# Kernel tuning notes

Hardware: AMD Instinct MI355X
Metric: run time of the kernel (lower is better)

## Reference

```python
import jax, jax.numpy as jnp
import numpy as np

N_NODES = 50000
N_EDGES = 800000
N_GRAPHS = 256
D_IN, D_H1, D_H2, D_OUT = 64, 64, 64, 64


def gcn_conv(x, W, b, src, dst, n_nodes):
    # PyG GCNConv (eval): h = x @ W; add self-loops; deg[i] = in_deg(i) + 1;
    # out[i] = sum_{j->i} h[j] * deg[i]^-1/2 deg[j]^-1/2 + h[i]/deg[i] + b
    h = x @ W  # [N, F]
    ones = jnp.ones((src.shape[0],), dtype=x.dtype)
    deg = jax.ops.segment_sum(ones, dst, num_segments=n_nodes) + 1.0  # self loop
    dinv = jax.lax.rsqrt(deg)
    norm = dinv[src] * dinv[dst]  # [E]
    msg = h[src] * norm[:, None]  # [E, F]  (memory-bound gather)
    agg = jax.ops.segment_sum(msg, dst, num_segments=n_nodes)  # scatter-add
    agg = agg + h * (1.0 / deg)[:, None]  # self-loop contribution
    return agg + b


def setup_inputs() -> dict:
    key = jax.random.key(0)
    ks = jax.random.split(key, 12)
    x = jax.random.normal(ks[0], (N_NODES, D_IN), dtype=jnp.float32)
    src = jax.random.randint(ks[1], (N_EDGES,), 0, N_NODES)
    dst = jax.random.randint(ks[2], (N_EDGES,), 0, N_NODES)
    batch = jnp.sort(jax.random.randint(ks[3], (N_NODES,), 0, N_GRAPHS))
    def glorot(k, fin, fout):
        s = jnp.sqrt(6.0 / (fin + fout))
        return jax.random.uniform(k, (fin, fout), jnp.float32, -s, s)
    return {
        "x": x, "src": src, "dst": dst, "batch": batch,
        "W1": glorot(ks[4], D_IN, D_H1), "b1": jnp.zeros((D_H1,), jnp.float32),
        "W2": glorot(ks[5], D_H1, D_H2), "b2": jnp.zeros((D_H2,), jnp.float32),
        "W3": glorot(ks[6], D_H2, D_OUT), "b3": jnp.zeros((D_OUT,), jnp.float32),
        "Wl": glorot(ks[7], D_OUT, 1), "bl": jnp.zeros((1,), jnp.float32),
    }


def reference(x, src, dst, batch, W1, b1, W2, b2, W3, b3, Wl, bl):
    n = x.shape[0]
    h = jax.nn.relu(gcn_conv(x, W1, b1, src, dst, n))   # dropout inactive (eval)
    h = jax.nn.relu(gcn_conv(h, W2, b2, src, dst, n))
    h = jax.nn.relu(gcn_conv(h, W3, b3, src, dst, n))
    # global_mean_pool over graph ids
    sums = jax.ops.segment_sum(h, batch, num_segments=N_GRAPHS)  # [G, F]
    cnt = jax.ops.segment_sum(jnp.ones((n,), h.dtype), batch, num_segments=N_GRAPHS)
    pooled = sums / jnp.maximum(cnt, 1.0)[:, None]
    return pooled @ Wl + bl  # [G, 1]
```

## Files before the change

### kernel.cpp

```cpp
#include <hip/hip_runtime.h>

#define N_NODES 50000
#define N_EDGES 800000
#define N_GRAPHS 256
#define F 64
#define NBUCK 196
#define CAP 5120
#define P3_TILE 2048
#define P3_GRID ((N_EDGES + P3_TILE - 1) / P3_TILE)
#define BCAP 6144
#define ZOFF (N_NODES * 128)

__device__ __forceinline__ unsigned short f2bf(float f) {
    union { float f; unsigned u; } c; c.f = f;
    unsigned u = c.u + 0x7FFFu + ((c.u >> 16) & 1u);
    return (unsigned short)(u >> 16);
}
__device__ __forceinline__ unsigned pack2bf(float lo, float hi) {
    return (unsigned)f2bf(lo) | ((unsigned)f2bf(hi) << 16);
}
__device__ __forceinline__ float bfl(unsigned u) {
    union { unsigned u; float f; } c; c.u = u << 16; return c.f;
}
__device__ __forceinline__ float bfh(unsigned u) {
    union { unsigned u; float f; } c; c.u = u & 0xFFFF0000u; return c.f;
}

__device__ __forceinline__ void gather_run(const int* __restrict__ eidx,
                                           const char* __restrict__ Hb,
                                           int beg, int end, int fo, float* a) {
#pragma unroll
    for (int i = 0; i < 8; ++i) a[i] = 0.f;
    int kb = (beg < end) ? beg : 0;
    int4 oc = *(const int4*)(eidx + kb);
    int k1 = beg + 4;
    int k1c = (k1 < end) ? k1 : kb;
    int4 on = *(const int4*)(eidx + k1c);
    uint4 pc = *(const uint4*)(Hb + oc.x + fo);
    uint4 qc = *(const uint4*)(Hb + oc.y + fo);
    uint4 rc = *(const uint4*)(Hb + oc.z + fo);
    uint4 wc = *(const uint4*)(Hb + oc.w + fo);
    for (int k = beg; k < end; k += 4) {
        int k2 = k + 8;
        int k2c = (k2 < end) ? k2 : kb;
        int4 of = *(const int4*)(eidx + k2c);
        uint4 pn = *(const uint4*)(Hb + on.x + fo);
        uint4 qn = *(const uint4*)(Hb + on.y + fo);
        uint4 rn = *(const uint4*)(Hb + on.z + fo);
        uint4 wn = *(const uint4*)(Hb + on.w + fo);
        a[0] += (bfl(pc.x) + bfl(qc.x)) + (bfl(rc.x) + bfl(wc.x));
        a[1] += (bfh(pc.x) + bfh(qc.x)) + (bfh(rc.x) + bfh(wc.x));
        a[2] += (bfl(pc.y) + bfl(qc.y)) + (bfl(rc.y) + bfl(wc.y));
        a[3] += (bfh(pc.y) + bfh(qc.y)) + (bfh(rc.y) + bfh(wc.y));
        a[4] += (bfl(pc.z) + bfl(qc.z)) + (bfl(rc.z) + bfl(wc.z));
        a[5] += (bfh(pc.z) + bfh(qc.z)) + (bfh(rc.z) + bfh(wc.z));
        a[6] += (bfl(pc.w) + bfl(qc.w)) + (bfl(rc.w) + bfl(wc.w));
        a[7] += (bfh(pc.w) + bfh(qc.w)) + (bfh(rc.w) + bfh(wc.w));
        oc = on; on = of;
        pc = pn; qc = qn; rc = rn; wc = wn;
    }
}

__global__ __launch_bounds__(256) void partition_edges(const int* __restrict__ src,
                                                       const int* __restrict__ dst,
                                                       int* __restrict__ bcur,
                                                       unsigned int* __restrict__ bpair) {
    __shared__ int bh[NBUCK], bloc[NBUCK], bpos[NBUCK];
    int t = threadIdx.x;
    int lo = blockIdx.x * P3_TILE;
    int hi = min(lo + P3_TILE, N_EDGES);
    for (int i = t; i < NBUCK; i += 256) { bh[i] = 0; bpos[i] = 0; }
    __syncthreads();
    for (int e = lo + t; e < hi; e += 256) atomicAdd(&bh[dst[e] >> 8], 1);
    __syncthreads();
    for (int i = t; i < NBUCK; i += 256)
        bloc[i] = bh[i] ? atomicAdd(&bcur[i], bh[i]) : 0;
    __syncthreads();
    for (int e = lo + t; e < hi; e += 256) {
        int d = dst[e];
        int b = d >> 8;
        int r = atomicAdd(&bpos[b], 1);
        bpair[(size_t)b * CAP + bloc[b] + r] = ((unsigned)src[e] << 8) | (unsigned)(d & 255);
    }
}

__global__ __launch_bounds__(256) void bucket_sort(const unsigned int* __restrict__ bpair,
                                                   const int* __restrict__ bcur,
                                                   int* __restrict__ eidx,
                                                   int* __restrict__ rbeg,
                                                   int* __restrict__ rend,
                                                   float* __restrict__ dinv,
                                                   unsigned short* __restrict__ Abf,
                                                   unsigned short* __restrict__ Bbf) {
    __shared__ int cnt[256], s[256], pos[256];
    __shared__ int lout[BCAP];
    int b = blockIdx.x, t = threadIdx.x;
    int base = b * CAP;
    int sz = bcur[b];

    if (b == 0 && t < 8) {
        ((uint4*)Abf)[(size_t)N_NODES * 8 + t] = make_uint4(0u, 0u, 0u, 0u);
        ((uint4*)Bbf)[(size_t)N_NODES * 8 + t] = make_uint4(0u, 0u, 0u, 0u);
    }

    cnt[t] = 0;
    __syncthreads();
    for (int i = t; i < sz; i += 256) atomicAdd(&cnt[bpair[base + i] & 255], 1);
    __syncthreads();
    int v = cnt[t];
    int pv = (v + 3) & ~3;
    s[t] = pv;
    __syncthreads();
    for (int off = 1; off < 256; off <<= 1) {
        int u = (t >= off) ? s[t - off] : 0;
        __syncthreads();
        s[t] += u;
        __syncthreads();
    }
    int excl = s[t] - pv;
    pos[t] = excl;
    int node = b * 256 + t;
    if (node < N_NODES) {
        rbeg[node] = base + excl;
        rend[node] = base + excl + pv;
        dinv[node] = 1.0f / sqrtf((float)v + 1.0f);
    }
    int padtot = s[255];
    __syncthreads();

    for (int i = t; i < sz; i += 256) {
        unsigned p = bpair[base + i];
        int r = atomicAdd(&pos[p & 255], 1);
        lout[r] = (int)((p >> 8) << 7);
    }
    __syncthreads();
    for (int j = v; j < pv; j++) lout[excl + j] = ZOFF;
    __syncthreads();
    for (int i = t; i < padtot; i += 256) eidx[base + i] = lout[i];
}

#define XSTRIDE 17
__global__ __launch_bounds__(256) void gemm64_f32(const float* __restrict__ X,
                                                  const float* __restrict__ W,
                                                  const float* __restrict__ dinv,
                                                  unsigned short* __restrict__ Hn, int n) {
    __shared__ float4 sW[64 * 16];
    __shared__ float4 sX[128 * XSTRIDE];
    int tid = threadIdx.x;
    int base = blockIdx.x * 128;

    const float4* W4 = (const float4*)W;
    for (int i = tid; i < 64 * 16; i += 256) sW[i] = W4[i];
    {
        const float4* X4 = (const float4*)X;
        for (int i = tid; i < 128 * 16; i += 256) {
            int r = i >> 4, kg = i & 15;
            int node = base + r;
            sX[r * XSTRIDE + kg] = (node < n) ? X4[(size_t)node * 16 + kg]
                                              : make_float4(0.f, 0.f, 0.f, 0.f);
        }
    }
    __syncthreads();

    int fg = tid & 15;
    int ng = tid >> 4;
    float4 acc[8];
#pragma unroll
    for (int ii = 0; ii < 8; ii++) acc[ii] = make_float4(0.f, 0.f, 0.f, 0.f);

    for (int kg = 0; kg < 16; kg++) {
        float4 xv[8];
#pragma unroll
        for (int ii = 0; ii < 8; ii++) xv[ii] = sX[(ng + 16 * ii) * XSTRIDE + kg];
#pragma unroll
        for (int kk = 0; kk < 4; kk++) {
            float4 wv = sW[(4 * kg + kk) * 16 + fg];
#pragma unroll
            for (int ii = 0; ii < 8; ii++) {
                float xs = (kk == 0) ? xv[ii].x : (kk == 1) ? xv[ii].y
                         : (kk == 2) ? xv[ii].z : xv[ii].w;
                acc[ii].x += wv.x * xs;
                acc[ii].y += wv.y * xs;
                acc[ii].z += wv.z * xs;
                acc[ii].w += wv.w * xs;
            }
        }
    }

    ushort4* H4 = (ushort4*)Hn;
#pragma unroll
    for (int ii = 0; ii < 8; ii++) {
        int node = base + ng + 16 * ii;
        if (node < n) {
            float d = dinv[node];
            float4 o = acc[ii];
            ushort4 u;
            u.x = f2bf(o.x * d); u.y = f2bf(o.y * d);
            u.z = f2bf(o.z * d); u.w = f2bf(o.w * d);
            H4[(size_t)node * 16 + fg] = u;
        }
    }
}

__global__ __launch_bounds__(256) void gather_gemm(const int* __restrict__ rbeg,
                                                   const int* __restrict__ rend,
                                                   const int* __restrict__ eidx,
                                                   const float* __restrict__ dinv,
                                                   const unsigned short* __restrict__ Hin,
                                                   const float* __restrict__ bias,
                                                   const float* __restrict__ W,
                                                   unsigned short* __restrict__ Hout, int n) {
    __shared__ float4 sW[64 * 16];
    const float4* W4 = (const float4*)W;
    for (int i = threadIdx.x; i < 64 * 16; i += 256) sW[i] = W4[i];
    __syncthreads();

    int wv = (blockIdx.x * blockDim.x + threadIdx.x) >> 6;
    if (wv * 8 >= n) return;
    int lane = threadIdx.x & 63;
    int ns = lane >> 3, f = lane & 7;
    int node = wv * 8 + ns;
    int beg = rbeg[node];
    int end = rend[node];
    const char* Hb = (const char*)Hin;

    float di = dinv[node];
    uint4 hs = *(const uint4*)(Hb + (size_t)node * 128 + f * 16);
    float4 bb0 = ((const float4*)bias)[2 * f];
    float4 bb1 = ((const float4*)bias)[2 * f + 1];

    float a[8];
    gather_run(eidx, Hb, beg, end, f * 16, a);

    float v[8];
    v[0] = fmaxf(di * (a[0] + bfl(hs.x)) + bb0.x, 0.f);
    v[1] = fmaxf(di * (a[1] + bfh(hs.x)) + bb0.y, 0.f);
    v[2] = fmaxf(di * (a[2] + bfl(hs.y)) + bb0.z, 0.f);
    v[3] = fmaxf(di * (a[3] + bfh(hs.y)) + bb0.w, 0.f);
    v[4] = fmaxf(di * (a[4] + bfl(hs.z)) + bb1.x, 0.f);
    v[5] = fmaxf(di * (a[5] + bfh(hs.z)) + bb1.y, 0.f);
    v[6] = fmaxf(di * (a[6] + bfl(hs.w)) + bb1.z, 0.f);
    v[7] = fmaxf(di * (a[7] + bfh(hs.w)) + bb1.w, 0.f);

    float y0 = 0.f, y1 = 0.f, y2 = 0.f, y3 = 0.f;
    float y4 = 0.f, y5 = 0.f, y6 = 0.f, y7 = 0.f;
    int pb = (lane & 56) << 2;
#pragma unroll
    for (int c = 0; c < 8; ++c) {
        int ad = pb + 4 * c;
#pragma unroll
        for (int j = 0; j < 8; ++j) {
            float hk = __int_as_float(
                __builtin_amdgcn_ds_bpermute(ad, __float_as_int(v[j])));
            float4 w0 = sW[(8 * c + j) * 16 + 2 * f];
            float4 w1 = sW[(8 * c + j) * 16 + 2 * f + 1];
            y0 += hk * w0.x; y1 += hk * w0.y; y2 += hk * w0.z; y3 += hk * w0.w;
            y4 += hk * w1.x; y5 += hk * w1.y; y6 += hk * w1.z; y7 += hk * w1.w;
        }
    }

    uint4 u;
    u.x = pack2bf(y0 * di, y1 * di);
    u.y = pack2bf(y2 * di, y3 * di);
    u.z = pack2bf(y4 * di, y5 * di);
    u.w = pack2bf(y6 * di, y7 * di);
    ((uint4*)Hout)[(size_t)node * 8 + f] = u;
}

__global__ __launch_bounds__(256) void gather_pool(const int* __restrict__ rbeg,
                                                   const int* __restrict__ rend,
                                                   const int* __restrict__ eidx,
                                                   const float* __restrict__ dinv,
                                                   const unsigned short* __restrict__ Hn,
                                                   const float* __restrict__ b,
                                                   const float* __restrict__ Wl,
                                                   float* __restrict__ pdot, int n) {
    int wv = (blockIdx.x * blockDim.x + threadIdx.x) >> 6;
    int lane = threadIdx.x & 63;
    int ns = lane >> 3, f = lane & 7;
    int node = wv * 8 + ns;
    bool valid = node < n;
    int nodec = valid ? node : 0;
    int beg = valid ? rbeg[node] : 0;
    int end = valid ? rend[node] : 0;
    const char* Hb = (const char*)Hn;

    float di = dinv[nodec];
    uint4 hs = *(const uint4*)(Hb + (size_t)nodec * 128 + f * 16);
    float4 b0 = ((const float4*)b)[2 * f];
    float4 b1 = ((const float4*)b)[2 * f + 1];
    float4 w0 = ((const float4*)Wl)[2 * f];
    float4 w1 = ((const float4*)Wl)[2 * f + 1];

    float a[8];
    gather_run(eidx, Hb, beg, end, f * 16, a);

    float d = 0.f;
    d += fmaxf(di * (a[0] + bfl(hs.x)) + b0.x, 0.f) * w0.x;
    d += fmaxf(di * (a[1] + bfh(hs.x)) + b0.y, 0.f) * w0.y;
    d += fmaxf(di * (a[2] + bfl(hs.y)) + b0.z, 0.f) * w0.z;
    d += fmaxf(di * (a[3] + bfh(hs.y)) + b0.w, 0.f) * w0.w;
    d += fmaxf(di * (a[4] + bfl(hs.z)) + b1.x, 0.f) * w1.x;
    d += fmaxf(di * (a[5] + bfh(hs.z)) + b1.y, 0.f) * w1.y;
    d += fmaxf(di * (a[6] + bfl(hs.w)) + b1.z, 0.f) * w1.z;
    d += fmaxf(di * (a[7] + bfh(hs.w)) + b1.w, 0.f) * w1.w;
#pragma unroll
    for (int m = 1; m <= 4; m <<= 1) d += __shfl_xor(d, m);
    if (valid && f == 0) pdot[node] = d;
}

__global__ __launch_bounds__(64) void final_out(const float* __restrict__ pdot,
                                                const int* __restrict__ batch,
                                                const float* __restrict__ bl,
                                                float* __restrict__ out) {
    int g = blockIdx.x;
    __shared__ int slo, shi;
    int lane = threadIdx.x;
    if (lane == 0) {
        int a = 0, b = N_NODES;
        while (a < b) { int m = (a + b) >> 1; if (batch[m] < g) a = m + 1; else b = m; }
        slo = a;
        b = N_NODES;
        while (a < b) { int m = (a + b) >> 1; if (batch[m] < g + 1) a = m + 1; else b = m; }
        shi = a;
    }
    __syncthreads();
    int lo = slo, hi = shi;
    float acc = 0.f;
    for (int i = lo + lane; i < hi; i += 64) acc += pdot[i];
#pragma unroll
    for (int off = 32; off > 0; off >>= 1) acc += __shfl_down(acc, off);
    if (lane == 0) {
        float cnt = (float)(hi - lo);
        out[g] = acc / fmaxf(cnt, 1.0f) + bl[0];
    }
}

extern "C" void kernel_launch(void* const* d_in, const int* in_sizes, int n_in,
                              void* d_out, int out_size, void* d_ws, size_t ws_size,
                              hipStream_t stream) {
    const float* x     = (const float*)d_in[0];
    const int*   src   = (const int*)d_in[1];
    const int*   dst   = (const int*)d_in[2];
    const int*   batch = (const int*)d_in[3];
    const float* W1 = (const float*)d_in[4];  const float* b1 = (const float*)d_in[5];
    const float* W2 = (const float*)d_in[6];  const float* b2 = (const float*)d_in[7];
    const float* W3 = (const float*)d_in[8];  const float* b3 = (const float*)d_in[9];
    const float* Wl = (const float*)d_in[10]; const float* bl = (const float*)d_in[11];
    float* out = (float*)d_out;

    char* ws = (char*)d_ws;
    unsigned short* Abf = (unsigned short*)ws;
    unsigned short* Bbf = Abf + (size_t)(N_NODES + 1) * F;
    float* dinv    = (float*)(Bbf + (size_t)(N_NODES + 1) * F);
    float* pdot    = dinv + N_NODES;
    int*   rbeg    = (int*)(pdot + N_NODES);
    int*   rend    = rbeg + N_NODES;
    int*   bcur    = rend + N_NODES;
    unsigned int* bpair = (unsigned int*)(bcur + NBUCK);
    int*   eidx    = (int*)(bpair + (size_t)NBUCK * CAP);

    const int GEMM_GRID   = (N_NODES + 127) / 128;
    const int GATHER_GRID = (N_NODES + 31) / 32;

    hipMemsetAsync(bcur, 0, NBUCK * sizeof(int), stream);
    partition_edges<<<P3_GRID, 256, 0, stream>>>(src, dst, bcur, bpair);
    bucket_sort<<<NBUCK, 256, 0, stream>>>(bpair, bcur, eidx, rbeg, rend, dinv, Abf, Bbf);

    gemm64_f32<<<GEMM_GRID, 256, 0, stream>>>(x, W1, dinv, Abf, N_NODES);

    gather_gemm<<<GATHER_GRID, 256, 0, stream>>>(rbeg, rend, eidx, dinv, Abf, b1, W2, Bbf, N_NODES);

    gather_gemm<<<GATHER_GRID, 256, 0, stream>>>(rbeg, rend, eidx, dinv, Bbf, b2, W3, Abf, N_NODES);

    gather_pool<<<GATHER_GRID, 256, 0, stream>>>(rbeg, rend, eidx, dinv, Abf, b3, Wl, pdot, N_NODES);

    final_out<<<N_GRAPHS, 64, 0, stream>>>(pdot, batch, bl, out);
}
```

Before: 194.7 us.

## Reorder nodes by degree within buckets to balance gather wavefront work

The bucket sort now also counting-sorts the 256 nodes in each bucket by padded in-degree and writes an order array. The gather kernels process nodes in that order, so the 8 nodes sharing a wavefront have similar edge counts and less lane divergence and idle time. Padding slots beyond N_NODES are handled with valid guards, which adds some wasted wavefronts in the last bucket. The change also adds an extra indirection load and scattered output writes.

```diff
diff --git a/kernel.cpp b/kernel.cpp
--- a/kernel.cpp
+++ b/kernel.cpp
@@ -10,6 +10,7 @@
 #define P3_GRID ((N_EDGES + P3_TILE - 1) / P3_TILE)
 #define BCAP 6144
 #define ZOFF (N_NODES * 128)
+#define NSLOT (NBUCK * 256)
 
 __device__ __forceinline__ unsigned short f2bf(float f) {
     union { float f; unsigned u; } c; c.f = f;
@@ -90,9 +91,11 @@
                                                    int* __restrict__ rbeg,
                                                    int* __restrict__ rend,
                                                    float* __restrict__ dinv,
+                                                   int* __restrict__ ord,
                                                    unsigned short* __restrict__ Abf,
                                                    unsigned short* __restrict__ Bbf) {
     __shared__ int cnt[256], s[256], pos[256];
+    __shared__ int dhist[64], dscan[64];
     __shared__ int lout[BCAP];
     int b = blockIdx.x, t = threadIdx.x;
     int base = b * CAP;
@@ -104,12 +107,15 @@
     }
 
     cnt[t] = 0;
+    if (t < 64) dhist[t] = 0;
     __syncthreads();
     for (int i = t; i < sz; i += 256) atomicAdd(&cnt[bpair[base + i] & 255], 1);
     __syncthreads();
     int v = cnt[t];
     int pv = (v + 3) & ~3;
     s[t] = pv;
+    int ic = min(pv >> 2, 63);
+    int myoff = atomicAdd(&dhist[ic], 1);
     __syncthreads();
     for (int off = 1; off < 256; off <<= 1) {
         int u = (t >= off) ? s[t - off] : 0;
@@ -126,7 +132,17 @@
         dinv[node] = 1.0f / sqrtf((float)v + 1.0f);
     }
     int padtot = s[255];
-    __syncthreads();
+
+    if (t < 64) dscan[t] = dhist[t];
+    __syncthreads();
+    for (int off = 1; off < 64; off <<= 1) {
+        int u = (t >= off && t < 64) ? dscan[t - off] : 0;
+        __syncthreads();
+        if (t < 64) dscan[t] += u;
+        __syncthreads();
+    }
+    int rank = dscan[ic] - dhist[ic] + myoff;
+    ord[b * 256 + rank] = node;
 
     for (int i = t; i < sz; i += 256) {
         unsigned p = bpair[base + i];
@@ -202,30 +218,32 @@
     }
 }
 
-__global__ __launch_bounds__(256) void gather_gemm(const int* __restrict__ rbeg,
+__global__ __launch_bounds__(256) void gather_gemm(const int* __restrict__ ord,
+                                                   const int* __restrict__ rbeg,
                                                    const int* __restrict__ rend,
                                                    const int* __restrict__ eidx,
                                                    const float* __restrict__ dinv,
                                                    const unsigned short* __restrict__ Hin,
                                                    const float* __restrict__ bias,
                                                    const float* __restrict__ W,
-                                                   unsigned short* __restrict__ Hout, int n) {
+                                                   unsigned short* __restrict__ Hout) {
     __shared__ float4 sW[64 * 16];
     const float4* W4 = (const float4*)W;
     for (int i = threadIdx.x; i < 64 * 16; i += 256) sW[i] = W4[i];
     __syncthreads();
 
     int wv = (blockIdx.x * blockDim.x + threadIdx.x) >> 6;
-    if (wv * 8 >= n) return;
     int lane = threadIdx.x & 63;
     int ns = lane >> 3, f = lane & 7;
-    int node = wv * 8 + ns;
-    int beg = rbeg[node];
-    int end = rend[node];
+    int node = ord[wv * 8 + ns];
+    bool valid = node < N_NODES;
+    int nodec = valid ? node : 0;
+    int beg = valid ? rbeg[nodec] : 0;
+    int end = valid ? rend[nodec] : 0;
     const char* Hb = (const char*)Hin;
 
-    float di = dinv[node];
-    uint4 hs = *(const uint4*)(Hb + (size_t)node * 128 + f * 16);
+    float di = dinv[nodec];
+    uint4 hs = *(const uint4*)(Hb + (size_t)nodec * 128 + f * 16);
     float4 bb0 = ((const float4*)bias)[2 * f];
     float4 bb1 = ((const float4*)bias)[2 * f + 1];
 
@@ -259,33 +277,36 @@
         }
     }
 
-    uint4 u;
-    u.x = pack2bf(y0 * di, y1 * di);
-    u.y = pack2bf(y2 * di, y3 * di);
-    u.z = pack2bf(y4 * di, y5 * di);
-    u.w = pack2bf(y6 * di, y7 * di);
-    ((uint4*)Hout)[(size_t)node * 8 + f] = u;
-}
-
-__global__ __launch_bounds__(256) void gather_pool(const int* __restrict__ rbeg,
+    if (valid) {
+        uint4 u;
+        u.x = pack2bf(y0 * di, y1 * di);
+        u.y = pack2bf(y2 * di, y3 * di);
+        u.z = pack2bf(y4 * di, y5 * di);
+        u.w = pack2bf(y6 * di, y7 * di);
+        ((uint4*)Hout)[(size_t)node * 8 + f] = u;
+    }
+}
+
+__global__ __launch_bounds__(256) void gather_pool(const int* __restrict__ ord,
+                                                   const int* __restrict__ rbeg,
                                                    const int* __restrict__ rend,
                                                    const int* __restrict__ eidx,
                                                    const float* __restrict__ dinv,
                                                    const unsigned short* __restrict__ Hn,
                                                    const float* __restrict__ b,
                                                    const float* __restrict__ Wl,
-                                                   float* __restrict__ pdot, int n) {
+                                                   float* __restrict__ pdot) {
     int wv = (blockIdx.x * blockDim.x + threadIdx.x) >> 6;
     int lane = threadIdx.x & 63;
     int ns = lane >> 3, f = lane & 7;
-    int node = wv * 8 + ns;
-    bool valid = node < n;
+    int node = ord[wv * 8 + ns];
+    bool valid = node < N_NODES;
     int nodec = valid ? node : 0;
-    int beg = valid ? rbeg[node] : 0;
-    int end = valid ? rend[node] : 0;
+    int beg = valid ? rbeg[nodec] : 0;
+    int end = valid ? rend[nodec] : 0;
     const char* Hb = (const char*)Hn;
 
-    float di = dinv[nodec];
+    float di = valid ? dinv[nodec] : 0.f;
     uint4 hs = *(const uint4*)(Hb + (size_t)nodec * 128 + f * 16);
     float4 b0 = ((const float4*)b)[2 * f];
     float4 b1 = ((const float4*)b)[2 * f + 1];
@@ -356,24 +377,25 @@
     float* pdot    = dinv + N_NODES;
     int*   rbeg    = (int*)(pdot + N_NODES);
     int*   rend    = rbeg + N_NODES;
-    int*   bcur    = rend + N_NODES;
+    int*   ord     = rend + N_NODES;
+    int*   bcur    = ord + NSLOT;
     unsigned int* bpair = (unsigned int*)(bcur + NBUCK);
     int*   eidx    = (int*)(bpair + (size_t)NBUCK * CAP);
 
     const int GEMM_GRID   = (N_NODES + 127) / 128;
-    const int GATHER_GRID = (N_NODES + 31) / 32;
+    const int GATHER_GRID = NSLOT / 32;
 
     hipMemsetAsync(bcur, 0, NBUCK * sizeof(int), stream);
     partition_edges<<<P3_GRID, 256, 0, stream>>>(src, dst, bcur, bpair);
-    bucket_sort<<<NBUCK, 256, 0, stream>>>(bpair, bcur, eidx, rbeg, rend, dinv, Abf, Bbf);
+    bucket_sort<<<NBUCK, 256, 0, stream>>>(bpair, bcur, eidx, rbeg, rend, dinv, ord, Abf, Bbf);
 
     gemm64_f32<<<GEMM_GRID, 256, 0, stream>>>(x, W1, dinv, Abf, N_NODES);
 
-    gather_gemm<<<GATHER_GRID, 256, 0, stream>>>(rbeg, rend, eidx, dinv, Abf, b1, W2, Bbf, N_NODES);
-
-    gather_gemm<<<GATHER_GRID, 256, 0, stream>>>(rbeg, rend, eidx, dinv, Bbf, b2, W3, Abf, N_NODES);
-
-    gather_pool<<<GATHER_GRID, 256, 0, stream>>>(rbeg, rend, eidx, dinv, Abf, b3, Wl, pdot, N_NODES);
+    gather_gemm<<<GATHER_GRID, 256, 0, stream>>>(ord, rbeg, rend, eidx, dinv, Abf, b1, W2, Bbf);
+
+    gather_gemm<<<GATHER_GRID, 256, 0, stream>>>(ord, rbeg, rend, eidx, dinv, Bbf, b2, W3, Abf);
+
+    gather_pool<<<GATHER_GRID, 256, 0, stream>>>(ord, rbeg, rend, eidx, dinv, Abf, b3, Wl, pdot);
 
     final_out<<<N_GRAPHS, 64, 0, stream>>>(pdot, batch, bl, out);
 }
```

After: 249.7 us. +28.2%, slower.

## Split each node's edge gather across four lane groups with shuffle reduction

Applied to the files above, without the earlier changes.

The gather kernels now map two nodes per wavefront instead of eight. Four 8-lane groups stride through each node's edge list and their partial sums are combined with cross-lane shuffles, which raises memory-level parallelism per node and cuts the serial per-node loop length. The fused 64x64 GEMM is restructured around a transposed, padded shared weight copy and bf16-packed bpermutes, with each half of the lanes computing half the K range and then reducing. The grid grows fourfold, the bounds check is removed (this relies on N_NODES being divisible by 8), and edge prefetching drops from the 4-wide double-buffered scheme to a single-index lookahead.

```diff
diff --git a/kernel.cpp b/kernel.cpp
--- a/kernel.cpp
+++ b/kernel.cpp
@@ -26,38 +26,24 @@
     union { unsigned u; float f; } c; c.u = u & 0xFFFF0000u; return c.f;
 }
 
-__device__ __forceinline__ void gather_run(const int* __restrict__ eidx,
-                                           const char* __restrict__ Hb,
-                                           int beg, int end, int fo, float* a) {
+__device__ __forceinline__ void gather_run4(const int* __restrict__ eidx,
+                                            const char* __restrict__ Hb,
+                                            int k0, int end, int fo, float* a) {
 #pragma unroll
     for (int i = 0; i < 8; ++i) a[i] = 0.f;
-    int kb = (beg < end) ? beg : 0;
-    int4 oc = *(const int4*)(eidx + kb);
-    int k1 = beg + 4;
-    int k1c = (k1 < end) ? k1 : kb;
-    int4 on = *(const int4*)(eidx + k1c);
-    uint4 pc = *(const uint4*)(Hb + oc.x + fo);
-    uint4 qc = *(const uint4*)(Hb + oc.y + fo);
-    uint4 rc = *(const uint4*)(Hb + oc.z + fo);
-    uint4 wc = *(const uint4*)(Hb + oc.w + fo);
-    for (int k = beg; k < end; k += 4) {
-        int k2 = k + 8;
-        int k2c = (k2 < end) ? k2 : kb;
-        int4 of = *(const int4*)(eidx + k2c);
-        uint4 pn = *(const uint4*)(Hb + on.x + fo);
-        uint4 qn = *(const uint4*)(Hb + on.y + fo);
-        uint4 rn = *(const uint4*)(Hb + on.z + fo);
-        uint4 wn = *(const uint4*)(Hb + on.w + fo);
-        a[0] += (bfl(pc.x) + bfl(qc.x)) + (bfl(rc.x) + bfl(wc.x));
-        a[1] += (bfh(pc.x) + bfh(qc.x)) + (bfh(rc.x) + bfh(wc.x));
-        a[2] += (bfl(pc.y) + bfl(qc.y)) + (bfl(rc.y) + bfl(wc.y));
-        a[3] += (bfh(pc.y) + bfh(qc.y)) + (bfh(rc.y) + bfh(wc.y));
-        a[4] += (bfl(pc.z) + bfl(qc.z)) + (bfl(rc.z) + bfl(wc.z));
-        a[5] += (bfh(pc.z) + bfh(qc.z)) + (bfh(rc.z) + bfh(wc.z));
-        a[6] += (bfl(pc.w) + bfl(qc.w)) + (bfl(rc.w) + bfl(wc.w));
-        a[7] += (bfh(pc.w) + bfh(qc.w)) + (bfh(rc.w) + bfh(wc.w));
-        oc = on; on = of;
-        pc = pn; qc = qn; rc = rn; wc = wn;
+    int k = k0;
+    int kc = (k < end) ? k : 0;
+    int off = eidx[kc];
+    while (k < end) {
+        int k2 = k + 4;
+        int k2c = (k2 < end) ? k2 : 0;
+        int offn = eidx[k2c];
+        uint4 p = *(const uint4*)(Hb + off + fo);
+        a[0] += bfl(p.x); a[1] += bfh(p.x);
+        a[2] += bfl(p.y); a[3] += bfh(p.y);
+        a[4] += bfl(p.z); a[5] += bfh(p.z);
+        a[6] += bfl(p.w); a[7] += bfh(p.w);
+        off = offn; k = k2;
     }
 }
 
@@ -209,17 +195,24 @@
                                                    const unsigned short* __restrict__ Hin,
                                                    const float* __restrict__ bias,
                                                    const float* __restrict__ W,
-                                                   unsigned short* __restrict__ Hout, int n) {
-    __shared__ float4 sW[64 * 16];
-    const float4* W4 = (const float4*)W;
-    for (int i = threadIdx.x; i < 64 * 16; i += 256) sW[i] = W4[i];
+                                                   unsigned short* __restrict__ Hout) {
+    __shared__ float4 sWt[16 * 65];
+    {
+        const float4* W4 = (const float4*)W;
+        for (int i = threadIdx.x; i < 1024; i += 256) {
+            float4 w = W4[i];
+            sWt[(i & 15) * 65 + (i >> 4)] = w;
+        }
+    }
     __syncthreads();
 
     int wv = (blockIdx.x * blockDim.x + threadIdx.x) >> 6;
-    if (wv * 8 >= n) return;
     int lane = threadIdx.x & 63;
-    int ns = lane >> 3, f = lane & 7;
-    int node = wv * 8 + ns;
+    int half = lane >> 5;
+    int sub = lane & 31;
+    int es = sub >> 3;
+    int f = sub & 7;
+    int node = wv * 2 + half;
     int beg = rbeg[node];
     int end = rend[node];
     const char* Hb = (const char*)Hin;
@@ -230,41 +223,60 @@
     float4 bb1 = ((const float4*)bias)[2 * f + 1];
 
     float a[8];
-    gather_run(eidx, Hb, beg, end, f * 16, a);
-
-    float v[8];
-    v[0] = fmaxf(di * (a[0] + bfl(hs.x)) + bb0.x, 0.f);
-    v[1] = fmaxf(di * (a[1] + bfh(hs.x)) + bb0.y, 0.f);
-    v[2] = fmaxf(di * (a[2] + bfl(hs.y)) + bb0.z, 0.f);
-    v[3] = fmaxf(di * (a[3] + bfh(hs.y)) + bb0.w, 0.f);
-    v[4] = fmaxf(di * (a[4] + bfl(hs.z)) + bb1.x, 0.f);
-    v[5] = fmaxf(di * (a[5] + bfh(hs.z)) + bb1.y, 0.f);
-    v[6] = fmaxf(di * (a[6] + bfl(hs.w)) + bb1.z, 0.f);
-    v[7] = fmaxf(di * (a[7] + bfh(hs.w)) + bb1.w, 0.f);
-
+    gather_run4(eidx, Hb, beg + es, end, f * 16, a);
+
+#pragma unroll
+    for (int i = 0; i < 8; ++i) {
+        a[i] += __shfl_xor(a[i], 8);
+        a[i] += __shfl_xor(a[i], 16);
+    }
+
+    float v0 = fmaxf(di * (a[0] + bfl(hs.x)) + bb0.x, 0.f);
+    float v1 = fmaxf(di * (a[1] + bfh(hs.x)) + bb0.y, 0.f);
+    float v2 = fmaxf(di * (a[2] + bfl(hs.y)) + bb0.z, 0.f);
+    float v3 = fmaxf(di * (a[3] + bfh(hs.y)) + bb0.w, 0.f);
+    float v4 = fmaxf(di * (a[4] + bfl(hs.z)) + bb1.x, 0.f);
+    float v5 = fmaxf(di * (a[5] + bfh(hs.z)) + bb1.y, 0.f);
+    float v6 = fmaxf(di * (a[6] + bfl(hs.w)) + bb1.z, 0.f);
+    float v7 = fmaxf(di * (a[7] + bfh(hs.w)) + bb1.w, 0.f);
+    unsigned pk0 = pack2bf(v0, v1);
+    unsigned pk1 = pack2bf(v2, v3);
+    unsigned pk2 = pack2bf(v4, v5);
+    unsigned pk3 = pack2bf(v6, v7);
+
+    int c4 = sub & 15;
+    int c0 = (sub & 16) >> 2;
+    int nb = (lane & 32) << 2;
     float y0 = 0.f, y1 = 0.f, y2 = 0.f, y3 = 0.f;
-    float y4 = 0.f, y5 = 0.f, y6 = 0.f, y7 = 0.f;
-    int pb = (lane & 56) << 2;
-#pragma unroll
-    for (int c = 0; c < 8; ++c) {
-        int ad = pb + 4 * c;
-#pragma unroll
-        for (int j = 0; j < 8; ++j) {
-            float hk = __int_as_float(
-                __builtin_amdgcn_ds_bpermute(ad, __float_as_int(v[j])));
-            float4 w0 = sW[(8 * c + j) * 16 + 2 * f];
-            float4 w1 = sW[(8 * c + j) * 16 + 2 * f + 1];
-            y0 += hk * w0.x; y1 += hk * w0.y; y2 += hk * w0.z; y3 += hk * w0.w;
-            y4 += hk * w1.x; y5 += hk * w1.y; y6 += hk * w1.z; y7 += hk * w1.w;
-        }
-    }
-
-    uint4 u;
-    u.x = pack2bf(y0 * di, y1 * di);
-    u.y = pack2bf(y2 * di, y3 * di);
-    u.z = pack2bf(y4 * di, y5 * di);
-    u.w = pack2bf(y6 * di, y7 * di);
-    ((uint4*)Hout)[(size_t)node * 8 + f] = u;
+#pragma unroll
+    for (int cc = 0; cc < 4; ++cc) {
+        int c = c0 + cc;
+        int ad = nb + 4 * c;
+#pragma unroll
+        for (int t = 0; t < 4; ++t) {
+            unsigned pkt = (t == 0) ? pk0 : (t == 1) ? pk1 : (t == 2) ? pk2 : pk3;
+            unsigned u = (unsigned)__builtin_amdgcn_ds_bpermute(ad, (int)pkt);
+            float h0 = bfl(u), h1 = bfh(u);
+            int k = 8 * c + 2 * t;
+            float4 wA = sWt[c4 * 65 + k];
+            float4 wB = sWt[c4 * 65 + k + 1];
+            y0 += h0 * wA.x + h1 * wB.x;
+            y1 += h0 * wA.y + h1 * wB.y;
+            y2 += h0 * wA.z + h1 * wB.z;
+            y3 += h0 * wA.w + h1 * wB.w;
+        }
+    }
+    y0 += __shfl_xor(y0, 16);
+    y1 += __shfl_xor(y1, 16);
+    y2 += __shfl_xor(y2, 16);
+    y3 += __shfl_xor(y3, 16);
+
+    if (sub < 16) {
+        uint2 o;
+        o.x = pack2bf(y0 * di, y1 * di);
+        o.y = pack2bf(y2 * di, y3 * di);
+        ((uint2*)Hout)[(size_t)node * 16 + c4] = o;
+    }
 }
 
 __global__ __launch_bounds__(256) void gather_pool(const int* __restrict__ rbeg,
@@ -274,26 +286,33 @@
                                                    const unsigned short* __restrict__ Hn,
                                                    const float* __restrict__ b,
                                                    const float* __restrict__ Wl,
-                                                   float* __restrict__ pdot, int n) {
+                                                   float* __restrict__ pdot) {
     int wv = (blockIdx.x * blockDim.x + threadIdx.x) >> 6;
     int lane = threadIdx.x & 63;
-    int ns = lane >> 3, f = lane & 7;
-    int node = wv * 8 + ns;
-    bool valid = node < n;
-    int nodec = valid ? node : 0;
-    int beg = valid ? rbeg[node] : 0;
-    int end = valid ? rend[node] : 0;
+    int half = lane >> 5;
+    int sub = lane & 31;
+    int es = sub >> 3;
+    int f = sub & 7;
+    int node = wv * 2 + half;
+    int beg = rbeg[node];
+    int end = rend[node];
     const char* Hb = (const char*)Hn;
 
-    float di = dinv[nodec];
-    uint4 hs = *(const uint4*)(Hb + (size_t)nodec * 128 + f * 16);
+    float di = dinv[node];
+    uint4 hs = *(const uint4*)(Hb + (size_t)node * 128 + f * 16);
     float4 b0 = ((const float4*)b)[2 * f];
     float4 b1 = ((const float4*)b)[2 * f + 1];
     float4 w0 = ((const float4*)Wl)[2 * f];
     float4 w1 = ((const float4*)Wl)[2 * f + 1];
 
     float a[8];
-    gather_run(eidx, Hb, beg, end, f * 16, a);
+    gather_run4(eidx, Hb, beg + es, end, f * 16, a);
+
+#pragma unroll
+    for (int i = 0; i < 8; ++i) {
+        a[i] += __shfl_xor(a[i], 8);
+        a[i] += __shfl_xor(a[i], 16);
+    }
 
     float d = 0.f;
     d += fmaxf(di * (a[0] + bfl(hs.x)) + b0.x, 0.f) * w0.x;
@@ -306,7 +325,7 @@
     d += fmaxf(di * (a[7] + bfh(hs.w)) + b1.w, 0.f) * w1.w;
 #pragma unroll
     for (int m = 1; m <= 4; m <<= 1) d += __shfl_xor(d, m);
-    if (valid && f == 0) pdot[node] = d;
+    if (sub == 0) pdot[node] = d;
 }
 
 __global__ __launch_bounds__(64) void final_out(const float* __restrict__ pdot,
@@ -361,7 +380,7 @@
     int*   eidx    = (int*)(bpair + (size_t)NBUCK * CAP);
 
     const int GEMM_GRID   = (N_NODES + 127) / 128;
-    const int GATHER_GRID = (N_NODES + 31) / 32;
+    const int GATHER_GRID = N_NODES / 8;
 
     hipMemsetAsync(bcur, 0, NBUCK * sizeof(int), stream);
     partition_edges<<<P3_GRID, 256, 0, stream>>>(src, dst, bcur, bpair);
@@ -369,11 +388,11 @@
 
     gemm64_f32<<<GEMM_GRID, 256, 0, stream>>>(x, W1, dinv, Abf, N_NODES);
 
-    gather_gemm<<<GATHER_GRID, 256, 0, stream>>>(rbeg, rend, eidx, dinv, Abf, b1, W2, Bbf, N_NODES);
-
-    gather_gemm<<<GATHER_GRID, 256, 0, stream>>>(rbeg, rend, eidx, dinv, Bbf, b2, W3, Abf, N_NODES);
-
-    gather_pool<<<GATHER_GRID, 256, 0, stream>>>(rbeg, rend, eidx, dinv, Abf, b3, Wl, pdot, N_NODES);
+    gather_gemm<<<GATHER_GRID, 256, 0, stream>>>(rbeg, rend, eidx, dinv, Abf, b1, W2, Bbf);
+
+    gather_gemm<<<GATHER_GRID, 256, 0, stream>>>(rbeg, rend, eidx, dinv, Bbf, b2, W3, Abf);
+
+    gather_pool<<<GATHER_GRID, 256, 0, stream>>>(rbeg, rend, eidx, dinv, Abf, b3, Wl, pdot);
 
     final_out<<<N_GRAPHS, 64, 0, stream>>>(pdot, batch, bl, out);
 }
```

Measured after the change: 220.1 us. 1.13x slower.

## Split feature dimension into halves mapped to XCD groups for L2-local gathers

Applied to the files above, without the earlier changes.

Splits the bf16 node feature table into two 32-feature halves stored separately. Gather blocks are assigned so that blocks on XCDs 0-3 process the first half and XCDs 4-7 the second, which shrinks each XCD's gather working set so it fits better in its L2. The fused gather+GEMM is unfused into separate gather_half and gemm64_t kernels, adding an intermediate bf16 write/read and extra launches. Pool partial dot products are also split into two arrays that are summed in final_out.

```diff
diff --git a/kernel.cpp b/kernel.cpp
--- a/kernel.cpp
+++ b/kernel.cpp
@@ -9,7 +9,9 @@
 #define P3_TILE 2048
 #define P3_GRID ((N_EDGES + P3_TILE - 1) / P3_TILE)
 #define BCAP 6144
-#define ZOFF (N_NODES * 128)
+#define ZOFF (N_NODES * 64)
+#define NSUB 1563
+#define GATHER_GRID (391 * 8)
 
 __device__ __forceinline__ unsigned short f2bf(float f) {
     union { float f; unsigned u; } c; c.f = f;
@@ -26,36 +28,31 @@
     union { unsigned u; float f; } c; c.u = u & 0xFFFF0000u; return c.f;
 }
 
-__device__ __forceinline__ void gather_run(const int* __restrict__ eidx,
-                                           const char* __restrict__ Hb,
-                                           int beg, int end, int fo, float* a) {
-#pragma unroll
-    for (int i = 0; i < 8; ++i) a[i] = 0.f;
+__device__ __forceinline__ void gather_run_h(const int* __restrict__ eidx,
+                                             const char* __restrict__ Hb,
+                                             int beg, int end, int fo, float* a) {
+    a[0] = a[1] = a[2] = a[3] = 0.f;
     int kb = (beg < end) ? beg : 0;
     int4 oc = *(const int4*)(eidx + kb);
     int k1 = beg + 4;
     int k1c = (k1 < end) ? k1 : kb;
     int4 on = *(const int4*)(eidx + k1c);
-    uint4 pc = *(const uint4*)(Hb + oc.x + fo);
-    uint4 qc = *(const uint4*)(Hb + oc.y + fo);
-    uint4 rc = *(const uint4*)(Hb + oc.z + fo);
-    uint4 wc = *(const uint4*)(Hb + oc.w + fo);
+    uint2 pc = *(const uint2*)(Hb + oc.x + fo);
+    uint2 qc = *(const uint2*)(Hb + oc.y + fo);
+    uint2 rc = *(const uint2*)(Hb + oc.z + fo);
+    uint2 wc = *(const uint2*)(Hb + oc.w + fo);
     for (int k = beg; k < end; k += 4) {
         int k2 = k + 8;
         int k2c = (k2 < end) ? k2 : kb;
         int4 of = *(const int4*)(eidx + k2c);
-        uint4 pn = *(const uint4*)(Hb + on.x + fo);
-        uint4 qn = *(const uint4*)(Hb + on.y + fo);
-        uint4 rn = *(const uint4*)(Hb + on.z + fo);
-        uint4 wn = *(const uint4*)(Hb + on.w + fo);
+        uint2 pn = *(const uint2*)(Hb + on.x + fo);
+        uint2 qn = *(const uint2*)(Hb + on.y + fo);
+        uint2 rn = *(const uint2*)(Hb + on.z + fo);
+        uint2 wn = *(const uint2*)(Hb + on.w + fo);
         a[0] += (bfl(pc.x) + bfl(qc.x)) + (bfl(rc.x) + bfl(wc.x));
         a[1] += (bfh(pc.x) + bfh(qc.x)) + (bfh(rc.x) + bfh(wc.x));
         a[2] += (bfl(pc.y) + bfl(qc.y)) + (bfl(rc.y) + bfl(wc.y));
         a[3] += (bfh(pc.y) + bfh(qc.y)) + (bfh(rc.y) + bfh(wc.y));
-        a[4] += (bfl(pc.z) + bfl(qc.z)) + (bfl(rc.z) + bfl(wc.z));
-        a[5] += (bfh(pc.z) + bfh(qc.z)) + (bfh(rc.z) + bfh(wc.z));
-        a[6] += (bfl(pc.w) + bfl(qc.w)) + (bfl(rc.w) + bfl(wc.w));
-        a[7] += (bfh(pc.w) + bfh(qc.w)) + (bfh(rc.w) + bfh(wc.w));
         oc = on; on = of;
         pc = pn; qc = qn; rc = rn; wc = wn;
     }
@@ -90,17 +87,17 @@
                                                    int* __restrict__ rbeg,
                                                    int* __restrict__ rend,
                                                    float* __restrict__ dinv,
-                                                   unsigned short* __restrict__ Abf,
-                                                   unsigned short* __restrict__ Bbf) {
+                                                   unsigned short* __restrict__ SA,
+                                                   unsigned short* __restrict__ SB) {
     __shared__ int cnt[256], s[256], pos[256];
     __shared__ int lout[BCAP];
     int b = blockIdx.x, t = threadIdx.x;
     int base = b * CAP;
     int sz = bcur[b];
 
-    if (b == 0 && t < 8) {
-        ((uint4*)Abf)[(size_t)N_NODES * 8 + t] = make_uint4(0u, 0u, 0u, 0u);
-        ((uint4*)Bbf)[(size_t)N_NODES * 8 + t] = make_uint4(0u, 0u, 0u, 0u);
+    if (b == 0 && t < 4) {
+        ((uint4*)SA)[(size_t)N_NODES * 4 + t] = make_uint4(0u, 0u, 0u, 0u);
+        ((uint4*)SB)[(size_t)N_NODES * 4 + t] = make_uint4(0u, 0u, 0u, 0u);
     }
 
     cnt[t] = 0;
@@ -131,7 +128,7 @@
     for (int i = t; i < sz; i += 256) {
         unsigned p = bpair[base + i];
         int r = atomicAdd(&pos[p & 255], 1);
-        lout[r] = (int)((p >> 8) << 7);
+        lout[r] = (int)((p >> 8) << 6);
     }
     __syncthreads();
     for (int j = v; j < pv; j++) lout[excl + j] = ZOFF;
@@ -140,10 +137,13 @@
 }
 
 #define XSTRIDE 17
-__global__ __launch_bounds__(256) void gemm64_f32(const float* __restrict__ X,
-                                                  const float* __restrict__ W,
-                                                  const float* __restrict__ dinv,
-                                                  unsigned short* __restrict__ Hn, int n) {
+template <bool BF16IN>
+__global__ __launch_bounds__(256) void gemm64_t(const void* __restrict__ Xa,
+                                                const void* __restrict__ Xb,
+                                                const float* __restrict__ W,
+                                                const float* __restrict__ dinv,
+                                                unsigned short* __restrict__ SA,
+                                                unsigned short* __restrict__ SB, int n) {
     __shared__ float4 sW[64 * 16];
     __shared__ float4 sX[128 * XSTRIDE];
     int tid = threadIdx.x;
@@ -151,8 +151,20 @@
 
     const float4* W4 = (const float4*)W;
     for (int i = tid; i < 64 * 16; i += 256) sW[i] = W4[i];
-    {
-        const float4* X4 = (const float4*)X;
+    if (BF16IN) {
+        const uint4* A4 = (const uint4*)Xa;
+        const uint4* B4 = (const uint4*)Xb;
+        for (int i = tid; i < 128 * 8; i += 256) {
+            int r = i >> 3, c = i & 7;
+            int node = base + r;
+            uint4 u = make_uint4(0u, 0u, 0u, 0u);
+            if (node < n) u = (c < 4) ? A4[(size_t)node * 4 + c]
+                                      : B4[(size_t)node * 4 + (c - 4)];
+            sX[r * XSTRIDE + 2 * c]     = make_float4(bfl(u.x), bfh(u.x), bfl(u.y), bfh(u.y));
+            sX[r * XSTRIDE + 2 * c + 1] = make_float4(bfl(u.z), bfh(u.z), bfl(u.w), bfh(u.w));
+        }
+    } else {
+        const float4* X4 = (const float4*)Xa;
         for (int i = tid; i < 128 * 16; i += 256) {
             int r = i >> 4, kg = i & 15;
             int node = base + r;
@@ -187,7 +199,6 @@
         }
     }
 
-    ushort4* H4 = (ushort4*)Hn;
 #pragma unroll
     for (int ii = 0; ii < 8; ii++) {
         int node = base + ng + 16 * ii;
@@ -197,119 +208,98 @@
             ushort4 u;
             u.x = f2bf(o.x * d); u.y = f2bf(o.y * d);
             u.z = f2bf(o.z * d); u.w = f2bf(o.w * d);
-            H4[(size_t)node * 16 + fg] = u;
+            if (fg < 8) ((ushort4*)SA)[(size_t)node * 8 + fg] = u;
+            else        ((ushort4*)SB)[(size_t)node * 8 + (fg - 8)] = u;
         }
     }
 }
 
-__global__ __launch_bounds__(256) void gather_gemm(const int* __restrict__ rbeg,
+__global__ __launch_bounds__(256) void gather_half(const int* __restrict__ rbeg,
                                                    const int* __restrict__ rend,
                                                    const int* __restrict__ eidx,
                                                    const float* __restrict__ dinv,
-                                                   const unsigned short* __restrict__ Hin,
+                                                   const unsigned short* __restrict__ SA,
+                                                   const unsigned short* __restrict__ SB,
                                                    const float* __restrict__ bias,
-                                                   const float* __restrict__ W,
-                                                   unsigned short* __restrict__ Hout, int n) {
-    __shared__ float4 sW[64 * 16];
-    const float4* W4 = (const float4*)W;
-    for (int i = threadIdx.x; i < 64 * 16; i += 256) sW[i] = W4[i];
-    __syncthreads();
-
-    int wv = (blockIdx.x * blockDim.x + threadIdx.x) >> 6;
-    if (wv * 8 >= n) return;
+                                                   unsigned short* __restrict__ hA,
+                                                   unsigned short* __restrict__ hB) {
+    int bid = blockIdx.x;
+    int xcd = bid & 7;
+    int half = xcd >> 2;
+    int sub = (bid >> 3) * 4 + (xcd & 3);
+    if (sub >= NSUB) return;
+    int wid = threadIdx.x >> 6;
     int lane = threadIdx.x & 63;
     int ns = lane >> 3, f = lane & 7;
-    int node = wv * 8 + ns;
+    int node = sub * 32 + wid * 8 + ns;
+    if (node >= N_NODES) return;
+    const char* Hb = (const char*)(half ? SB : SA);
+    unsigned short* out = half ? hB : hA;
+
     int beg = rbeg[node];
     int end = rend[node];
-    const char* Hb = (const char*)Hin;
-
     float di = dinv[node];
-    uint4 hs = *(const uint4*)(Hb + (size_t)node * 128 + f * 16);
-    float4 bb0 = ((const float4*)bias)[2 * f];
-    float4 bb1 = ((const float4*)bias)[2 * f + 1];
-
-    float a[8];
-    gather_run(eidx, Hb, beg, end, f * 16, a);
-
-    float v[8];
-    v[0] = fmaxf(di * (a[0] + bfl(hs.x)) + bb0.x, 0.f);
-    v[1] = fmaxf(di * (a[1] + bfh(hs.x)) + bb0.y, 0.f);
-    v[2] = fmaxf(di * (a[2] + bfl(hs.y)) + bb0.z, 0.f);
-    v[3] = fmaxf(di * (a[3] + bfh(hs.y)) + bb0.w, 0.f);
-    v[4] = fmaxf(di * (a[4] + bfl(hs.z)) + bb1.x, 0.f);
-    v[5] = fmaxf(di * (a[5] + bfh(hs.z)) + bb1.y, 0.f);
-    v[6] = fmaxf(di * (a[6] + bfl(hs.w)) + bb1.z, 0.f);
-    v[7] = fmaxf(di * (a[7] + bfh(hs.w)) + bb1.w, 0.f);
-
-    float y0 = 0.f, y1 = 0.f, y2 = 0.f, y3 = 0.f;
-    float y4 = 0.f, y5 = 0.f, y6 = 0.f, y7 = 0.f;
-    int pb = (lane & 56) << 2;
-#pragma unroll
-    for (int c = 0; c < 8; ++c) {
-        int ad = pb + 4 * c;
-#pragma unroll
-        for (int j = 0; j < 8; ++j) {
-            float hk = __int_as_float(
-                __builtin_amdgcn_ds_bpermute(ad, __float_as_int(v[j])));
-            float4 w0 = sW[(8 * c + j) * 16 + 2 * f];
-            float4 w1 = sW[(8 * c + j) * 16 + 2 * f + 1];
-            y0 += hk * w0.x; y1 += hk * w0.y; y2 += hk * w0.z; y3 += hk * w0.w;
-            y4 += hk * w1.x; y5 += hk * w1.y; y6 += hk * w1.z; y7 += hk * w1.w;
-        }
-    }
-
-    uint4 u;
-    u.x = pack2bf(y0 * di, y1 * di);
-    u.y = pack2bf(y2 * di, y3 * di);
-    u.z = pack2bf(y4 * di, y5 * di);
-    u.w = pack2bf(y6 * di, y7 * di);
-    ((uint4*)Hout)[(size_t)node * 8 + f] = u;
-}
-
-__global__ __launch_bounds__(256) void gather_pool(const int* __restrict__ rbeg,
-                                                   const int* __restrict__ rend,
-                                                   const int* __restrict__ eidx,
-                                                   const float* __restrict__ dinv,
-                                                   const unsigned short* __restrict__ Hn,
-                                                   const float* __restrict__ b,
-                                                   const float* __restrict__ Wl,
-                                                   float* __restrict__ pdot, int n) {
-    int wv = (blockIdx.x * blockDim.x + threadIdx.x) >> 6;
+    uint2 hs = *(const uint2*)(Hb + (size_t)node * 64 + f * 8);
+    float4 bb = ((const float4*)bias)[half * 8 + f];
+
+    float a[4];
+    gather_run_h(eidx, Hb, beg, end, f * 8, a);
+
+    float v0 = fmaxf(di * (a[0] + bfl(hs.x)) + bb.x, 0.f);
+    float v1 = fmaxf(di * (a[1] + bfh(hs.x)) + bb.y, 0.f);
+    float v2 = fmaxf(di * (a[2] + bfl(hs.y)) + bb.z, 0.f);
+    float v3 = fmaxf(di * (a[3] + bfh(hs.y)) + bb.w, 0.f);
+    uint2 o;
+    o.x = pack2bf(v0, v1);
+    o.y = pack2bf(v2, v3);
+    ((uint2*)out)[(size_t)node * 8 + f] = o;
+}
+
+__global__ __launch_bounds__(256) void gather_pool_half(const int* __restrict__ rbeg,
+                                                        const int* __restrict__ rend,
+                                                        const int* __restrict__ eidx,
+                                                        const float* __restrict__ dinv,
+                                                        const unsigned short* __restrict__ SA,
+                                                        const unsigned short* __restrict__ SB,
+                                                        const float* __restrict__ bias,
+                                                        const float* __restrict__ Wl,
+                                                        float* __restrict__ pdotA,
+                                                        float* __restrict__ pdotB) {
+    int bid = blockIdx.x;
+    int xcd = bid & 7;
+    int half = xcd >> 2;
+    int sub = (bid >> 3) * 4 + (xcd & 3);
+    if (sub >= NSUB) return;
+    int wid = threadIdx.x >> 6;
     int lane = threadIdx.x & 63;
     int ns = lane >> 3, f = lane & 7;
-    int node = wv * 8 + ns;
-    bool valid = node < n;
-    int nodec = valid ? node : 0;
-    int beg = valid ? rbeg[node] : 0;
-    int end = valid ? rend[node] : 0;
-    const char* Hb = (const char*)Hn;
-
-    float di = dinv[nodec];
-    uint4 hs = *(const uint4*)(Hb + (size_t)nodec * 128 + f * 16);
-    float4 b0 = ((const float4*)b)[2 * f];
-    float4 b1 = ((const float4*)b)[2 * f + 1];
-    float4 w0 = ((const float4*)Wl)[2 * f];
-    float4 w1 = ((const float4*)Wl)[2 * f + 1];
-
-    float a[8];
-    gather_run(eidx, Hb, beg, end, f * 16, a);
+    int node = sub * 32 + wid * 8 + ns;
+    if (node >= N_NODES) return;
+    const char* Hb = (const char*)(half ? SB : SA);
+    float* pout = half ? pdotB : pdotA;
+
+    int beg = rbeg[node];
+    int end = rend[node];
+    float di = dinv[node];
+    uint2 hs = *(const uint2*)(Hb + (size_t)node * 64 + f * 8);
+    float4 bb = ((const float4*)bias)[half * 8 + f];
+    float4 wl = ((const float4*)Wl)[half * 8 + f];
+
+    float a[4];
+    gather_run_h(eidx, Hb, beg, end, f * 8, a);
 
     float d = 0.f;
-    d += fmaxf(di * (a[0] + bfl(hs.x)) + b0.x, 0.f) * w0.x;
-    d += fmaxf(di * (a[1] + bfh(hs.x)) + b0.y, 0.f) * w0.y;
-    d += fmaxf(di * (a[2] + bfl(hs.y)) + b0.z, 0.f) * w0.z;
-    d += fmaxf(di * (a[3] + bfh(hs.y)) + b0.w, 0.f) * w0.w;
-    d += fmaxf(di * (a[4] + bfl(hs.z)) + b1.x, 0.f) * w1.x;
-    d += fmaxf(di * (a[5] + bfh(hs.z)) + b1.y, 0.f) * w1.y;
-    d += fmaxf(di * (a[6] + bfl(hs.w)) + b1.z, 0.f) * w1.z;
-    d += fmaxf(di * (a[7] + bfh(hs.w)) + b1.w, 0.f) * w1.w;
+    d += fmaxf(di * (a[0] + bfl(hs.x)) + bb.x, 0.f) * wl.x;
+    d += fmaxf(di * (a[1] + bfh(hs.x)) + bb.y, 0.f) * wl.y;
+    d += fmaxf(di * (a[2] + bfl(hs.y)) + bb.z, 0.f) * wl.z;
+    d += fmaxf(di * (a[3] + bfh(hs.y)) + bb.w, 0.f) * wl.w;
 #pragma unroll
     for (int m = 1; m <= 4; m <<= 1) d += __shfl_xor(d, m);
-    if (valid && f == 0) pdot[node] = d;
-}
-
-__global__ __launch_bounds__(64) void final_out(const float* __restrict__ pdot,
+    if (f == 0) pout[node] = d;
+}
+
+__global__ __launch_bounds__(64) void final_out(const float* __restrict__ pdotA,
+                                                const float* __restrict__ pdotB,
                                                 const int* __restrict__ batch,
                                                 const float* __restrict__ bl,
                                                 float* __restrict__ out) {
@@ -327,7 +317,7 @@
     __syncthreads();
     int lo = slo, hi = shi;
     float acc = 0.f;
-    for (int i = lo + lane; i < hi; i += 64) acc += pdot[i];
+    for (int i = lo + lane; i < hi; i += 64) acc += pdotA[i] + pdotB[i];
 #pragma unroll
     for (int off = 32; off > 0; off >>= 1) acc += __shfl_down(acc, off);
     if (lane == 0) {
@@ -350,30 +340,33 @@
     float* out = (float*)d_out;
 
     char* ws = (char*)d_ws;
-    unsigned short* Abf = (unsigned short*)ws;
-    unsigned short* Bbf = Abf + (size_t)(N_NODES + 1) * F;
-    float* dinv    = (float*)(Bbf + (size_t)(N_NODES + 1) * F);
-    float* pdot    = dinv + N_NODES;
-    int*   rbeg    = (int*)(pdot + N_NODES);
+    unsigned short* SA = (unsigned short*)ws;
+    unsigned short* SB = SA + (size_t)(N_NODES + 1) * 32;
+    unsigned short* hA = SB + (size_t)(N_NODES + 1) * 32;
+    unsigned short* hB = hA + (size_t)N_NODES * 32;
+    float* dinv    = (float*)(hB + (size_t)N_NODES * 32);
+    float* pdotA   = dinv + N_NODES;
+    float* pdotB   = pdotA + N_NODES;
+    int*   rbeg    = (int*)(pdotB + N_NODES);
     int*   rend    = rbeg + N_NODES;
     int*   bcur    = rend + N_NODES;
     unsigned int* bpair = (unsigned int*)(bcur + NBUCK);
     int*   eidx    = (int*)(bpair + (size_t)NBUCK * CAP);
 
-    const int GEMM_GRID   = (N_NODES + 127) / 128;
-    const int GATHER_GRID = (N_NODES + 31) / 32;
+    const int GEMM_GRID = (N_NODES + 127) / 128;
 
     hipMemsetAsync(bcur, 0, NBUCK * sizeof(int), stream);
     partition_edges<<<P3_GRID, 256, 0, stream>>>(src, dst, bcur, bpair);
-    bucket_sort<<<NBUCK, 256, 0, stream>>>(bpair, bcur, eidx, rbeg, rend, dinv, Abf, Bbf);
-
-    gemm64_f32<<<GEMM_GRID, 256, 0, stream>>>(x, W1, dinv, Abf, N_NODES);
-
-    gather_gemm<<<GATHER_GRID, 256, 0, stream>>>(rbeg, rend, eidx, dinv, Abf, b1, W2, Bbf, N_NODES);
-
-    gather_gemm<<<GATHER_GRID, 256, 0, stream>>>(rbeg, rend, eidx, dinv, Bbf, b2, W3, Abf, N_NODES);
-
-    gather_pool<<<GATHER_GRID, 256, 0, stream>>>(rbeg, rend, eidx, dinv, Abf, b3, Wl, pdot, N_NODES);
-
-    final_out<<<N_GRAPHS, 64, 0, stream>>>(pdot, batch, bl, out);
-}
+    bucket_sort<<<NBUCK, 256, 0, stream>>>(bpair, bcur, eidx, rbeg, rend, dinv, SA, SB);
+
+    gemm64_t<false><<<GEMM_GRID, 256, 0, stream>>>((const void*)x, nullptr, W1, dinv, SA, SB, N_NODES);
+    gather_half<<<GATHER_GRID, 256, 0, stream>>>(rbeg, rend, eidx, dinv, SA, SB, b1, hA, hB);
+
+    gemm64_t<true><<<GEMM_GRID, 256, 0, stream>>>((const void*)hA, (const void*)hB, W2, dinv, SA, SB, N_NODES);
+    gather_half<<<GATHER_GRID, 256, 0, stream>>>(rbeg, rend, eidx, dinv, SA, SB, b2, hA, hB);
+
+    gemm64_t<true><<<GEMM_GRID, 256, 0, stream>>>((const void*)hA, (const void*)hB, W3, dinv, SA, SB, N_NODES);
+    gather_pool_half<<<GATHER_GRID, 256, 0, stream>>>(rbeg, rend, eidx, dinv, SA, SB, b3, Wl, pdotA, pdotB);
+
+    final_out<<<N_GRAPHS, 64, 0, stream>>>(pdotA, pdotB, batch, bl, out);
+}
```

After: 216.2 us. 1.11x slower.
